# Performance work log

Hardware: AMD Instinct MI355X
Metric: run time of the kernel (lower is better)

The kernel has to match this reference:

```python
import jax, jax.numpy as jnp
import numpy as np

N_NODES = 100000
D = 128
ATT = 128
P_EDGE_TYPES = 3
N_EDGES = 1600000
BATCH = 65536


def gcn_conv(x, W, b, src, dst, n):
    # PyG GCNConv: add self loops, symmetric D^{-1/2} (A+I) D^{-1/2} x W + b
    h = x @ W                                   # [N, D]
    ones = jnp.ones(src.shape[0], x.dtype)
    deg = jax.ops.segment_sum(ones, dst, num_segments=n) + 1.0  # +1 self loop
    dinv = jax.lax.rsqrt(deg)
    norm = dinv[src] * dinv[dst]                # [E]
    out = jax.ops.segment_sum(h[src] * norm[:, None], dst, num_segments=n)
    out = out + h * (dinv * dinv)[:, None]      # self-loop message, norm = dinv_i^2
    return out + b


def semantic_attention(z, P, W, b, q):
    # z: [P*N, D] -> per-edge-type scalar attention, softmax over P, weighted sum
    att = jnp.tanh(z @ W + b) @ q               # [P*N]
    att = att.reshape(P, -1).mean(axis=1)       # [P]
    att = jax.nn.softmax(att)
    zp = z.reshape(P, -1, z.shape[-1])          # [P, N, D]
    return jnp.einsum('p,pnd->nd', att, zp)     # [N, D]


def gnn_branch(x0, edge_index, W1, b1, W2, b2, n):
    outs = []
    for t in range(edge_index.shape[0]):        # fixed small set of edge types
        src, dst = edge_index[t, 0], edge_index[t, 1]
        h = jax.nn.relu(gcn_conv(x0, W1, b1, src, dst, n))
        h = jax.nn.relu(gcn_conv(h, W2, b2, src, dst, n))
        outs.append(h)
    return jnp.concatenate(outs, axis=0)        # [P*N, D]


def setup_inputs() -> dict:
    key = jax.random.key(0)
    ks = jax.random.split(key, 16)
    x = jax.random.normal(ks[0], (N_NODES, D), jnp.float32)
    edge_index = jax.random.randint(ks[1], (P_EDGE_TYPES, 2, N_EDGES), 0, N_NODES, jnp.int64)
    perm = jax.random.permutation(ks[2], N_NODES).astype(jnp.int64)
    summary_vetor = jax.random.normal(ks[3], (D,), jnp.float32)
    s = 1.0 / np.sqrt(D)
    params = dict(
        W_lin=jax.random.normal(ks[4], (D, D), jnp.float32) * s,
        b_lin=jnp.zeros((D,), jnp.float32),
        W1=jax.random.normal(ks[5], (D, D), jnp.float32) * s,
        b1=jnp.zeros((D,), jnp.float32),
        W2=jax.random.normal(ks[6], (D, D), jnp.float32) * s,
        b2=jnp.zeros((D,), jnp.float32),
        W_sem=jax.random.normal(ks[7], (D, ATT), jnp.float32) * s,
        b_sem=jnp.zeros((ATT,), jnp.float32),
        q_sem=jax.random.normal(ks[8], (ATT,), jnp.float32) * (1.0 / np.sqrt(ATT)),
        W_disc=jax.random.normal(ks[9], (D, D), jnp.float32) * s,
        b_disc=jnp.zeros((), jnp.float32),
    )
    return dict(x=x, edge_index=edge_index, perm=perm,
                summary_vetor=summary_vetor, Batch_size=BATCH, **params)


def reference(x, edge_index, perm, summary_vetor, Batch_size,
              W_lin, b_lin, W1, b1, W2, b2, W_sem, b_sem, q_sem, W_disc, b_disc):
    n = x.shape[0]
    x_pos = jax.nn.relu(x @ W_lin + b_lin)
    x_neg = jax.nn.relu(x[perm] @ W_lin + b_lin)

    z_pos = gnn_branch(x_pos, edge_index, W1, b1, W2, b2, n)
    z_neg = gnn_branch(x_neg, edge_index, W1, b1, W2, b2, n)

    P = edge_index.shape[0]
    att_pos = semantic_attention(z_pos, P, W_sem, b_sem, q_sem)[:Batch_size]
    att_neg = semantic_attention(z_neg, P, W_sem, b_sem, q_sem)[:Batch_size]

    summary_in = att_pos.mean(axis=0)           # AvgReadout
    summary = 0.5 * (summary_vetor + summary_in)

    # Discriminator: bilinear score against broadcast summary
    c = W_disc @ summary                        # [D]
    sc_pos = att_pos @ c + b_disc               # [B]
    sc_neg = att_neg @ c + b_disc               # [B]
    ret = jnp.concatenate([sc_pos, sc_neg], axis=0)  # [2B]
    return ret, summary
```

## Files before the change

### kernel.cpp

```cpp
#include <hip/hip_runtime.h>

#define D_ 128
#define BATCH_ 65536
#define BSH 10
#define TILE_ 16384

typedef _Float16 f16;
typedef _Float16 h2v __attribute__((ext_vector_type(2)));
typedef _Float16 f16x8 __attribute__((ext_vector_type(8)));
typedef float f32x4 __attribute__((ext_vector_type(4)));

__global__ void k_zero32(uint32_t* p, long long n) {
    long long i = (long long)blockIdx.x * blockDim.x + threadIdx.x;
    long long st = (long long)gridDim.x * blockDim.x;
    for (; i < n; i += st) p[i] = 0u;
}

__global__ void k_sentinel(float* p, long long n) {
    long long i = (long long)blockIdx.x * blockDim.x + threadIdx.x;
    long long st = (long long)gridDim.x * blockDim.x;
    for (; i < n; i += st) p[i] = -12345.0f;
}

__global__ void k_wt(const float* __restrict__ W, f16* __restrict__ Wt) {
    int t = blockIdx.x * 256 + threadIdx.x;
    int k = t >> 7, c = t & 127;
    Wt[c * 128 + k] = (f16)W[k * 128 + c];
}

__global__ void k_gath(const uint32_t* __restrict__ src, const int* __restrict__ perm,
                       uint32_t* __restrict__ dst, int N) {
    int i = blockIdx.x * 256 + threadIdx.x;
    if (i >= N * 64) return;
    int row = i >> 6, col = i & 63;
    dst[i] = src[((size_t)perm[row] << 6) + col];
}

__global__ void k_hist(const int* __restrict__ ei, int* __restrict__ bcnt,
                       int E, int nbt, int nbuk) {
    __shared__ int hist[512];
    for (int i = threadIdx.x; i < 512; i += 256) hist[i] = 0;
    __syncthreads();
    long long tot = 3LL * E;
    long long i = (long long)blockIdx.x * 256 + threadIdx.x;
    long long st = (long long)gridDim.x * 256;
    for (; i < tot; i += st) {
        int t = (i >= E) + (i >= 2LL * E);
        long long w = i - (long long)t * E;
        int dst = ei[(long long)t * 2 * E + E + w];
        atomicAdd(&hist[t * nbt + (dst >> BSH)], 1);
    }
    __syncthreads();
    for (int i2 = threadIdx.x; i2 < nbuk; i2 += 256)
        if (hist[i2]) atomicAdd(&bcnt[i2], hist[i2]);
}

__global__ void k_bscan(const int* __restrict__ bcnt, int* __restrict__ bbase,
                        int* __restrict__ bcur, int nbuk) {
    __shared__ int s[512];
    int t = threadIdx.x;
    int v = (t < nbuk) ? bcnt[t] : 0;
    s[t] = v;
    __syncthreads();
    for (int off = 1; off < 512; off <<= 1) {
        int a = (t >= off) ? s[t - off] : 0;
        __syncthreads();
        s[t] += a;
        __syncthreads();
    }
    if (t < nbuk) {
        int e = s[t] - v;
        bbase[t] = e;
        bcur[t] = e;
        if (t == nbuk - 1) bbase[nbuk] = s[t];
    }
}

__global__ __launch_bounds__(256) void k_scatter(const int* __restrict__ ei,
                                                 int* __restrict__ bcur,
                                                 uint32_t* __restrict__ pairs,
                                                 int E, int nbt, int nbuk) {
    __shared__ int hist[512];
    __shared__ int base[512];
    long long tot = 3LL * E;
    long long w0 = (long long)blockIdx.x * TILE_;
    long long w1 = w0 + TILE_ < tot ? w0 + TILE_ : tot;
    for (int i = threadIdx.x; i < 512; i += 256) hist[i] = 0;
    __syncthreads();
    for (long long e = w0 + threadIdx.x; e < w1; e += 256) {
        int t = (e >= E) + (e >= 2LL * E);
        long long w = e - (long long)t * E;
        int dst = ei[(long long)t * 2 * E + E + w];
        atomicAdd(&hist[t * nbt + (dst >> BSH)], 1);
    }
    __syncthreads();
    for (int i = threadIdx.x; i < nbuk; i += 256) {
        int c = hist[i];
        base[i] = c ? atomicAdd(&bcur[i], c) : 0;
        hist[i] = 0;
    }
    __syncthreads();
    for (long long e = w0 + threadIdx.x; e < w1; e += 256) {
        int t = (e >= E) + (e >= 2LL * E);
        long long w = e - (long long)t * E;
        int src = ei[(long long)t * 2 * E + w];
        int dst = ei[(long long)t * 2 * E + E + w];
        int b = t * nbt + (dst >> BSH);
        int off = atomicAdd(&hist[b], 1);
        pairs[base[b] + off] = (uint32_t)src | ((uint32_t)(dst & ((1 << BSH) - 1)) << 22);
    }
}

__global__ __launch_bounds__(256) void k_bucket(const uint32_t* __restrict__ pairs,
                                                const int* __restrict__ bbase,
                                                int* __restrict__ rowstart,
                                                float* __restrict__ dinv,
                                                int* __restrict__ csr,
                                                int N, int nbt, int nbuk, int L) {
    __shared__ int cnt[1024];
    __shared__ int pref[1024];
    __shared__ int sums[256];
    int b = blockIdx.x;
    int t = b / nbt, bb = b - t * nbt;
    int dst0 = bb << BSH;
    int ndst = (N - dst0 < 1024) ? (N - dst0) : 1024;
    int e0 = bbase[b], e1 = bbase[b + 1];
    int tid = threadIdx.x;
    for (int i = tid; i < 1024; i += 256) cnt[i] = 0;
    __syncthreads();
    for (int e = e0 + tid; e < e1; e += 256) atomicAdd(&cnt[pairs[e] >> 22], 1);
    __syncthreads();
    int i0 = tid * 4;
    int c0 = cnt[i0], c1 = cnt[i0 + 1], c2 = cnt[i0 + 2], c3 = cnt[i0 + 3];
    int s4 = c0 + c1 + c2 + c3;
    sums[tid] = s4;
    __syncthreads();
    for (int off = 1; off < 256; off <<= 1) {
        int v = (tid >= off) ? sums[tid - off] : 0;
        __syncthreads();
        sums[tid] += v;
        __syncthreads();
    }
    int run = sums[tid] - s4;
    pref[i0] = run; run += c0;
    pref[i0 + 1] = run; run += c1;
    pref[i0 + 2] = run; run += c2;
    pref[i0 + 3] = run;
    __syncthreads();
    for (int d = tid; d < ndst; d += 256) {
        int r = t * N + dst0 + d;
        rowstart[r] = e0 + pref[d];
        dinv[r] = rsqrtf((float)cnt[d] + 1.0f);
    }
    if (b == nbuk - 1 && tid == 0) rowstart[L] = e1;
    __syncthreads();
    for (int e = e0 + tid; e < e1; e += 256) {
        uint32_t u = pairs[e];
        int d = u >> 22;
        int pos = e0 + atomicAdd(&pref[d], 1);
        csr[pos] = (int)(u & ((1u << 22) - 1));
    }
}

__global__ void k_wedge(const int* __restrict__ csr, const float* __restrict__ dinv,
                        f16* __restrict__ w16, int N, int E) {
    long long tot = 3LL * E;
    long long i = (long long)blockIdx.x * 256 + threadIdx.x;
    long long st = (long long)gridDim.x * 256;
    for (; i < tot; i += st) {
        int t = (i >= E) + (i >= 2LL * E);
        w16[i] = (f16)dinv[t * N + csr[i]];
    }
}

__global__ __launch_bounds__(256) void k_mgemm(const void* __restrict__ in, int in_f32,
                                               const f16* __restrict__ Wt,
                                               const float* __restrict__ bias,
                                               f16* __restrict__ outh, int n, int relu) {
    int l = threadIdx.x & 63, wid = threadIdx.x >> 6;
    int row0 = blockIdx.x * 128 + wid * 32;
    int r = l & 15, kg = l >> 4;
    f32x4 acc[2][8] = {};
#pragma unroll
    for (int kk = 0; kk < 4; kk++) {
        int off = kk * 32 + kg * 8;
        f16x8 a[2];
#pragma unroll
        for (int h = 0; h < 2; h++) {
            int arow = row0 + h * 16 + r;
            f16x8 av = {};
            if (arow < n) {
                if (in_f32) {
                    const float* inf = (const float*)in + (size_t)arow * D_ + off;
                    float4 v0 = *(const float4*)inf;
                    float4 v1 = *(const float4*)(inf + 4);
                    av[0] = (f16)v0.x; av[1] = (f16)v0.y; av[2] = (f16)v0.z; av[3] = (f16)v0.w;
                    av[4] = (f16)v1.x; av[5] = (f16)v1.y; av[6] = (f16)v1.z; av[7] = (f16)v1.w;
                } else {
                    av = *(const f16x8*)((const f16*)in + (size_t)arow * D_ + off);
                }
            }
            a[h] = av;
        }
#pragma unroll
        for (int ct = 0; ct < 8; ct++) {
            f16x8 b = *(const f16x8*)(Wt + (size_t)(ct * 16 + r) * D_ + off);
            acc[0][ct] = __builtin_amdgcn_mfma_f32_16x16x32_f16(a[0], b, acc[0][ct], 0, 0, 0);
            acc[1][ct] = __builtin_amdgcn_mfma_f32_16x16x32_f16(a[1], b, acc[1][ct], 0, 0, 0);
        }
    }
#pragma unroll
    for (int h = 0; h < 2; h++) {
#pragma unroll
        for (int ct = 0; ct < 8; ct++) {
            int c = ct * 16 + r;
            float bs = bias ? bias[c] : 0.0f;
#pragma unroll
            for (int j = 0; j < 4; j++) {
                int rr = row0 + h * 16 + kg * 4 + j;
                if (rr >= n) continue;
                float o = acc[h][ct][j] + bs;
                if (relu) o = fmaxf(o, 0.0f);
                outh[(size_t)rr * D_ + c] = (f16)o;
            }
        }
    }
}

__global__ __launch_bounds__(256) void k_matt(const f16* __restrict__ z,
                                              const f16* __restrict__ Wst,
                                              const float* __restrict__ bsem,
                                              const float* __restrict__ q,
                                              float* __restrict__ att_part, int N, int rows) {
    int l = threadIdx.x & 63, wid = threadIdx.x >> 6;
    int row0 = blockIdx.x * 128 + wid * 32;
    int r = l & 15, kg = l >> 4;
    f32x4 acc[2][8] = {};
#pragma unroll
    for (int kk = 0; kk < 4; kk++) {
        int off = kk * 32 + kg * 8;
        f16x8 a[2];
#pragma unroll
        for (int h = 0; h < 2; h++) {
            int arow = row0 + h * 16 + r;
            f16x8 av = {};
            if (arow < rows) av = *(const f16x8*)(z + (size_t)arow * D_ + off);
            a[h] = av;
        }
#pragma unroll
        for (int ct = 0; ct < 8; ct++) {
            f16x8 b = *(const f16x8*)(Wst + (size_t)(ct * 16 + r) * D_ + off);
            acc[0][ct] = __builtin_amdgcn_mfma_f32_16x16x32_f16(a[0], b, acc[0][ct], 0, 0, 0);
            acc[1][ct] = __builtin_amdgcn_mfma_f32_16x16x32_f16(a[1], b, acc[1][ct], 0, 0, 0);
        }
    }
#pragma unroll
    for (int h = 0; h < 2; h++) {
        int rowh = row0 + h * 16;
        if (rowh >= rows) continue;
        float s = 0.0f;
#pragma unroll
        for (int ct = 0; ct < 8; ct++) {
            int c = ct * 16 + r;
            float qc = q[c], bc = bsem[c];
#pragma unroll
            for (int j = 0; j < 4; j++) {
                int rr = rowh + kg * 4 + j;
                if (rr < rows) s += qc * tanhf(acc[h][ct][j] + bc);
            }
        }
#pragma unroll
        for (int m = 1; m < 64; m <<= 1) s += __shfl_xor(s, m, 64);
        if (l == 0) {
            int t = (rowh >= N) + (rowh >= 2 * N);
            atomicAdd(&att_part[((blockIdx.x & 63) << 2) + t], s);
        }
    }
}

__global__ __launch_bounds__(256) void k_spmm(const f16* __restrict__ gsrc,
                                              const int* __restrict__ csr,
                                              const f16* __restrict__ w16,
                                              const int* __restrict__ rowstart,
                                              const float* __restrict__ dinv,
                                              const float* __restrict__ bias,
                                              f16* __restrict__ outh,
                                              int N, int rows, int src_typed) {
    int tid = (int)threadIdx.x;
    int lp = tid & 15;
    int gw = blockIdx.x * 16 + (tid >> 4);
    if (gw >= rows) return;
    int t = (gw >= N) + (gw >= 2 * N);
    int tbase = t * N;
    int sbase = src_typed ? tbase : 0;
    int self = src_typed ? gw : gw - tbase;
    int s0 = rowstart[gw], s1 = rowstart[gw + 1];
    float di = dinv[gw];
    size_t co = (size_t)(lp << 3);
    const f16* gp = gsrc + co;
    float a[8];
    {
        f16x8 sv = *(const f16x8*)(gp + (size_t)self * D_);
#pragma unroll
        for (int u = 0; u < 8; u++) a[u] = (float)sv[u] * di;
    }
    int j = s0;
    for (; j + 2 <= s1; j += 2) {
        int sA = csr[j], sB = csr[j + 1];
        float wA = (float)w16[j], wB = (float)w16[j + 1];
        f16x8 vA = *(const f16x8*)(gp + (size_t)(sbase + sA) * D_);
        f16x8 vB = *(const f16x8*)(gp + (size_t)(sbase + sB) * D_);
#pragma unroll
        for (int u = 0; u < 8; u++) a[u] = fmaf((float)vA[u], wA, a[u]);
#pragma unroll
        for (int u = 0; u < 8; u++) a[u] = fmaf((float)vB[u], wB, a[u]);
    }
    if (j < s1) {
        int s = csr[j];
        float w = (float)w16[j];
        f16x8 v = *(const f16x8*)(gp + (size_t)(sbase + s) * D_);
#pragma unroll
        for (int u = 0; u < 8; u++) a[u] = fmaf((float)v[u], w, a[u]);
    }
    float4 b0 = *(const float4*)(bias + co);
    float4 b1 = *(const float4*)(bias + co + 4);
    f16x8 o;
    o[0] = (f16)fmaxf(fmaf(a[0], di, b0.x), 0.f);
    o[1] = (f16)fmaxf(fmaf(a[1], di, b0.y), 0.f);
    o[2] = (f16)fmaxf(fmaf(a[2], di, b0.z), 0.f);
    o[3] = (f16)fmaxf(fmaf(a[3], di, b0.w), 0.f);
    o[4] = (f16)fmaxf(fmaf(a[4], di, b1.x), 0.f);
    o[5] = (f16)fmaxf(fmaf(a[5], di, b1.y), 0.f);
    o[6] = (f16)fmaxf(fmaf(a[6], di, b1.z), 0.f);
    o[7] = (f16)fmaxf(fmaf(a[7], di, b1.w), 0.f);
    *(f16x8*)(outh + (size_t)gw * D_ + co) = o;
}

__global__ void k_attw(const float* __restrict__ att_part, float* __restrict__ att_w, float invN) {
    __shared__ float sb[3];
    int t = threadIdx.x;
    if (t < 3) {
        float s = 0.f;
        for (int i = 0; i < 64; i++) s += att_part[(i << 2) + t];
        sb[t] = s * invN;
    }
    __syncthreads();
    if (t == 0) {
        float m = fmaxf(sb[0], fmaxf(sb[1], sb[2]));
        float x0 = expf(sb[0] - m), x1 = expf(sb[1] - m), x2 = expf(sb[2] - m);
        float inv = 1.f / (x0 + x1 + x2);
        att_w[0] = x0 * inv; att_w[1] = x1 * inv; att_w[2] = x2 * inv;
    }
}

__global__ __launch_bounds__(256) void k_colsum(const f16* __restrict__ Z, size_t tstride,
                                                const float* __restrict__ att_w,
                                                float* __restrict__ colsum) {
    int c2 = threadIdx.x & 63;
    int rg = threadIdx.x >> 6;
    int nbase = blockIdx.x << 7;
    float w0 = att_w[0], w1 = att_w[1], w2 = att_w[2];
    float csx = 0.f, csy = 0.f;
    for (int i = rg; i < 128; i += 4) {
        size_t off = (size_t)(nbase + i) * D_ + (c2 << 1);
        h2v z0 = *(const h2v*)(Z + off);
        h2v z1 = *(const h2v*)(Z + tstride + off);
        h2v z2 = *(const h2v*)(Z + 2 * tstride + off);
        csx += w0 * (float)z0.x + w1 * (float)z1.x + w2 * (float)z2.x;
        csy += w0 * (float)z0.y + w1 * (float)z1.y + w2 * (float)z2.y;
    }
    __shared__ float red[4][128];
    red[rg][c2 << 1] = csx;
    red[rg][(c2 << 1) + 1] = csy;
    __syncthreads();
    if (rg == 0) {
        float sx = red[0][c2 << 1] + red[1][c2 << 1] + red[2][c2 << 1] + red[3][c2 << 1];
        float sy = red[0][(c2 << 1) + 1] + red[1][(c2 << 1) + 1] + red[2][(c2 << 1) + 1] + red[3][(c2 << 1) + 1];
        atomicAdd(&colsum[c2 << 1], sx);
        atomicAdd(&colsum[(c2 << 1) + 1], sy);
    }
}

__global__ void k_summary_c(const float* __restrict__ colsum, const float* __restrict__ sv,
                            const float* __restrict__ Wd, float* __restrict__ cvec,
                            float* __restrict__ out_summary) {
    __shared__ float sl[128];
    int t = threadIdx.x;
    float s = 0.5f * (sv[t] + colsum[t] * (1.0f / (float)BATCH_));
    sl[t] = s;
    out_summary[t] = s;
    __syncthreads();
    float a = 0.f;
    for (int j = 0; j < 128; j++) a = fmaf(Wd[t * D_ + j], sl[j], a);
    cvec[t] = a;
}

__global__ __launch_bounds__(256) void k_cscore(const f16* __restrict__ Z, size_t tstride,
                                                const float* __restrict__ att_w,
                                                const float* __restrict__ c,
                                                const float* __restrict__ bd,
                                                float* __restrict__ out, int B) {
    int gw = (int)((blockIdx.x * (long long)blockDim.x + threadIdx.x) >> 6);
    int lane = threadIdx.x & 63;
    if (gw >= B) return;
    size_t off = (size_t)gw * D_ + (lane << 1);
    float w0 = att_w[0], w1 = att_w[1], w2 = att_w[2];
    h2v z0 = *(const h2v*)(Z + off);
    h2v z1 = *(const h2v*)(Z + tstride + off);
    h2v z2 = *(const h2v*)(Z + 2 * tstride + off);
    float vx = w0 * (float)z0.x + w1 * (float)z1.x + w2 * (float)z2.x;
    float vy = w0 * (float)z0.y + w1 * (float)z1.y + w2 * (float)z2.y;
    float2 cc = *(const float2*)(c + (lane << 1));
    float a = vx * cc.x + vy * cc.y;
#pragma unroll
    for (int m = 1; m < 64; m <<= 1) a += __shfl_xor(a, m, 64);
    if (lane == 0) out[gw] = a + bd[0];
}

extern "C" void kernel_launch(void* const* d_in, const int* in_sizes, int n_in,
                              void* d_out, int out_size, void* d_ws, size_t ws_size,
                              hipStream_t stream) {
    const float* x      = (const float*)d_in[0];
    const int*   ei     = (const int*)d_in[1];
    const int*   perm   = (const int*)d_in[2];
    const float* sv     = (const float*)d_in[3];
    const float* W_lin  = (const float*)d_in[5];
    const float* b_lin  = (const float*)d_in[6];
    const float* W1     = (const float*)d_in[7];
    const float* b1     = (const float*)d_in[8];
    const float* W2     = (const float*)d_in[9];
    const float* b2     = (const float*)d_in[10];
    const float* W_sem  = (const float*)d_in[11];
    const float* b_sem  = (const float*)d_in[12];
    const float* q_sem  = (const float*)d_in[13];
    const float* W_disc = (const float*)d_in[14];
    const float* b_disc = (const float*)d_in[15];
    float* out = (float*)d_out;

    int N = in_sizes[0] / D_;
    int E = in_sizes[1] / 6;
    int L = 3 * N;
    size_t ND = (size_t)N * D_;
    int B = BATCH_;
    int nbt = (N + (1 << BSH) - 1) >> BSH;
    int nbuk = 3 * nbt;

    char* ws = (char*)d_ws;
    size_t o = 0;
    auto alloc = [&](size_t bytes) -> char* {
        char* p = ws + o;
        o = (o + bytes + 255) & ~(size_t)255;
        return p;
    };
    float* dinv     = (float*)alloc((size_t)L * 4);
    int*   rowstart = (int*)alloc(((size_t)L + 1) * 4);
    int*   csr      = (int*)alloc(((size_t)3 * E + 16) * 4);
    int*   bcnt     = (int*)alloc(512 * 4);
    int*   bbase    = (int*)alloc(513 * 4);
    int*   bcur     = (int*)alloc(512 * 4);
    float* att_part = (float*)alloc(256 * 4);
    float* att_w    = (float*)alloc(16 * 4);
    float* colsum   = (float*)alloc(128 * 4);
    float* cvec     = (float*)alloc(128 * 4);
    f16*   Wlt      = (f16*)alloc(128 * 128 * 2);
    f16*   W1t      = (f16*)alloc(128 * 128 * 2);
    f16*   W2t      = (f16*)alloc(128 * 128 * 2);
    f16*   Wst      = (f16*)alloc(128 * 128 * 2);
    f16*   Ah       = (f16*)alloc(ND * 2);
    f16*   G1h      = (f16*)alloc(ND * 2);
    f16*   G1p      = (f16*)alloc(ND * 2);
    f16*   H1all    = (f16*)alloc(3 * ND * 2);
    f16*   Zall     = (f16*)alloc(3 * ND * 2);
    size_t o_full = o;

    uint32_t* pairs = (uint32_t*)Zall;
    f16*      w16  = (f16*)Ah;

    if (o_full > ws_size || N >= (1 << 22) || (N & 15) || nbuk > 512 ||
        (size_t)3 * E * 4 > 3 * ND * 2 || (size_t)3 * E * 2 > ND * 2) {
        k_sentinel<<<256, 256, 0, stream>>>(out, out_size);
        return;
    }

    k_wt<<<64, 256, 0, stream>>>(W_lin, Wlt);
    k_wt<<<64, 256, 0, stream>>>(W1, W1t);
    k_wt<<<64, 256, 0, stream>>>(W2, W2t);
    k_wt<<<64, 256, 0, stream>>>(W_sem, Wst);

    long long tot = 3LL * E;
    k_zero32<<<2, 256, 0, stream>>>((uint32_t*)bcnt, 512);
    k_hist<<<2048, 256, 0, stream>>>(ei, bcnt, E, nbt, nbuk);
    k_bscan<<<1, 512, 0, stream>>>(bcnt, bbase, bcur, nbuk);
    int scat_grid = (int)((tot + TILE_ - 1) / TILE_);
    k_scatter<<<scat_grid, 256, 0, stream>>>(ei, bcur, pairs, E, nbt, nbuk);
    k_bucket<<<nbuk, 256, 0, stream>>>(pairs, bbase, rowstart, dinv, csr, N, nbt, nbuk, L);

    int mgN_grid  = (N + 127) / 128;
    int mgL_grid  = (L + 127) / 128;
    int spmm_grid = (L + 15) / 16;
    int scoreB_grid = (B + 3) / 4;

    k_mgemm<<<mgN_grid, 256, 0, stream>>>(x, 1, Wlt, b_lin, Ah, N, 1);
    k_mgemm<<<mgN_grid, 256, 0, stream>>>(Ah, 0, W1t, nullptr, G1h, N, 0);
    k_gath<<<(N * 64 + 255) / 256, 256, 0, stream>>>((const uint32_t*)G1h, perm,
                                                     (uint32_t*)G1p, N);
    k_wedge<<<2048, 256, 0, stream>>>(csr, dinv, w16, N, E);

    for (int br = 0; br < 2; br++) {
        const f16* src1 = br ? G1p : G1h;
        float* aw = att_w + br * 8;
        k_zero32<<<1, 256, 0, stream>>>((uint32_t*)att_part, 256);
        k_spmm<<<spmm_grid, 256, 0, stream>>>(src1, csr, w16, rowstart, dinv, b1,
                                              H1all, N, L, 0);
        k_mgemm<<<mgL_grid, 256, 0, stream>>>(H1all, 0, W2t, nullptr, H1all, L, 0);
        k_spmm<<<spmm_grid, 256, 0, stream>>>(H1all, csr, w16, rowstart, dinv, b2,
                                              Zall, N, L, 1);
        k_matt<<<mgL_grid, 256, 0, stream>>>(Zall, Wst, b_sem, q_sem, att_part, N, L);
        k_attw<<<1, 64, 0, stream>>>(att_part, aw, 1.0f / (float)N);
        if (br == 0) {
            k_zero32<<<1, 256, 0, stream>>>((uint32_t*)colsum, 128);
            k_colsum<<<512, 256, 0, stream>>>(Zall, ND, aw, colsum);
            k_summary_c<<<1, 128, 0, stream>>>(colsum, sv, W_disc, cvec, out + 2 * (size_t)B);
            k_cscore<<<scoreB_grid, 256, 0, stream>>>(Zall, ND, aw, cvec, b_disc, out, B);
        } else {
            k_cscore<<<scoreB_grid, 256, 0, stream>>>(Zall, ND, aw, cvec, b_disc, out + B, B);
        }
    }
}
```

Measured before the change: 1.411 ms.

## Fuse GEMM epilogues into SpMM kernels via shared-memory MFMA tiles

The first SpMM now writes its 16 aggregated rows to shared memory and multiplies them by W2 with MFMA in the same block, which removes the separate k_mgemm pass and the H1 round trip through global memory. The second SpMM likewise computes the semantic-attention GEMM, tanh and q-dot on its output tile and accumulates att_part, which removes the separate k_matt pass that re-read Zall. In exchange each 16-row block reloads the full 128x128 weight from global or L2, and the row-level SpMM now carries a block barrier plus extra register pressure from the MFMA phase.

```diff
diff --git a/kernel.cpp b/kernel.cpp
--- a/kernel.cpp
+++ b/kernel.cpp
@@ -227,113 +227,193 @@
     }
 }
 
-__global__ __launch_bounds__(256) void k_matt(const f16* __restrict__ z,
-                                              const f16* __restrict__ Wst,
-                                              const float* __restrict__ bsem,
-                                              const float* __restrict__ q,
-                                              float* __restrict__ att_part, int N, int rows) {
-    int l = threadIdx.x & 63, wid = threadIdx.x >> 6;
-    int row0 = blockIdx.x * 128 + wid * 32;
-    int r = l & 15, kg = l >> 4;
-    f32x4 acc[2][8] = {};
-#pragma unroll
-    for (int kk = 0; kk < 4; kk++) {
-        int off = kk * 32 + kg * 8;
-        f16x8 a[2];
-#pragma unroll
-        for (int h = 0; h < 2; h++) {
-            int arow = row0 + h * 16 + r;
-            f16x8 av = {};
-            if (arow < rows) av = *(const f16x8*)(z + (size_t)arow * D_ + off);
-            a[h] = av;
-        }
-#pragma unroll
-        for (int ct = 0; ct < 8; ct++) {
-            f16x8 b = *(const f16x8*)(Wst + (size_t)(ct * 16 + r) * D_ + off);
-            acc[0][ct] = __builtin_amdgcn_mfma_f32_16x16x32_f16(a[0], b, acc[0][ct], 0, 0, 0);
-            acc[1][ct] = __builtin_amdgcn_mfma_f32_16x16x32_f16(a[1], b, acc[1][ct], 0, 0, 0);
-        }
-    }
-#pragma unroll
-    for (int h = 0; h < 2; h++) {
-        int rowh = row0 + h * 16;
-        if (rowh >= rows) continue;
-        float s = 0.0f;
-#pragma unroll
-        for (int ct = 0; ct < 8; ct++) {
-            int c = ct * 16 + r;
-            float qc = q[c], bc = bsem[c];
-#pragma unroll
-            for (int j = 0; j < 4; j++) {
-                int rr = rowh + kg * 4 + j;
-                if (rr < rows) s += qc * tanhf(acc[h][ct][j] + bc);
-            }
-        }
-#pragma unroll
-        for (int m = 1; m < 64; m <<= 1) s += __shfl_xor(s, m, 64);
-        if (l == 0) {
-            int t = (rowh >= N) + (rowh >= 2 * N);
-            atomicAdd(&att_part[((blockIdx.x & 63) << 2) + t], s);
-        }
-    }
-}
-
-__global__ __launch_bounds__(256) void k_spmm(const f16* __restrict__ gsrc,
-                                              const int* __restrict__ csr,
-                                              const f16* __restrict__ w16,
-                                              const int* __restrict__ rowstart,
-                                              const float* __restrict__ dinv,
-                                              const float* __restrict__ bias,
-                                              f16* __restrict__ outh,
-                                              int N, int rows, int src_typed) {
+__global__ __launch_bounds__(256) void k_spmm1g(const f16* __restrict__ gsrc,
+                                                const int* __restrict__ csr,
+                                                const f16* __restrict__ w16,
+                                                const int* __restrict__ rowstart,
+                                                const float* __restrict__ dinv,
+                                                const float* __restrict__ bias,
+                                                const f16* __restrict__ Wt,
+                                                f16* __restrict__ outG,
+                                                int N, int rows, int src_typed) {
+    __shared__ f16 hs[16][136];
     int tid = (int)threadIdx.x;
     int lp = tid & 15;
-    int gw = blockIdx.x * 16 + (tid >> 4);
-    if (gw >= rows) return;
-    int t = (gw >= N) + (gw >= 2 * N);
-    int tbase = t * N;
-    int sbase = src_typed ? tbase : 0;
-    int self = src_typed ? gw : gw - tbase;
-    int s0 = rowstart[gw], s1 = rowstart[gw + 1];
-    float di = dinv[gw];
-    size_t co = (size_t)(lp << 3);
-    const f16* gp = gsrc + co;
-    float a[8];
-    {
-        f16x8 sv = *(const f16x8*)(gp + (size_t)self * D_);
-#pragma unroll
-        for (int u = 0; u < 8; u++) a[u] = (float)sv[u] * di;
-    }
-    int j = s0;
-    for (; j + 2 <= s1; j += 2) {
-        int sA = csr[j], sB = csr[j + 1];
-        float wA = (float)w16[j], wB = (float)w16[j + 1];
-        f16x8 vA = *(const f16x8*)(gp + (size_t)(sbase + sA) * D_);
-        f16x8 vB = *(const f16x8*)(gp + (size_t)(sbase + sB) * D_);
-#pragma unroll
-        for (int u = 0; u < 8; u++) a[u] = fmaf((float)vA[u], wA, a[u]);
-#pragma unroll
-        for (int u = 0; u < 8; u++) a[u] = fmaf((float)vB[u], wB, a[u]);
-    }
-    if (j < s1) {
-        int s = csr[j];
-        float w = (float)w16[j];
-        f16x8 v = *(const f16x8*)(gp + (size_t)(sbase + s) * D_);
-#pragma unroll
-        for (int u = 0; u < 8; u++) a[u] = fmaf((float)v[u], w, a[u]);
-    }
-    float4 b0 = *(const float4*)(bias + co);
-    float4 b1 = *(const float4*)(bias + co + 4);
-    f16x8 o;
-    o[0] = (f16)fmaxf(fmaf(a[0], di, b0.x), 0.f);
-    o[1] = (f16)fmaxf(fmaf(a[1], di, b0.y), 0.f);
-    o[2] = (f16)fmaxf(fmaf(a[2], di, b0.z), 0.f);
-    o[3] = (f16)fmaxf(fmaf(a[3], di, b0.w), 0.f);
-    o[4] = (f16)fmaxf(fmaf(a[4], di, b1.x), 0.f);
-    o[5] = (f16)fmaxf(fmaf(a[5], di, b1.y), 0.f);
-    o[6] = (f16)fmaxf(fmaf(a[6], di, b1.z), 0.f);
-    o[7] = (f16)fmaxf(fmaf(a[7], di, b1.w), 0.f);
-    *(f16x8*)(outh + (size_t)gw * D_ + co) = o;
+    int row16 = tid >> 4;
+    int gw0 = blockIdx.x * 16;
+    int gw = gw0 + row16;
+    bool valid = gw < rows;
+    float a[8] = {};
+    if (valid) {
+        int t = (gw >= N) + (gw >= 2 * N);
+        int tbase = t * N;
+        int sbase = src_typed ? tbase : 0;
+        int self = src_typed ? gw : gw - tbase;
+        int s0 = rowstart[gw], s1 = rowstart[gw + 1];
+        float di = dinv[gw];
+        size_t co = (size_t)(lp << 3);
+        const f16* gp = gsrc + co;
+        {
+            f16x8 sv = *(const f16x8*)(gp + (size_t)self * D_);
+#pragma unroll
+            for (int u = 0; u < 8; u++) a[u] = (float)sv[u] * di;
+        }
+        int j = s0;
+        for (; j + 2 <= s1; j += 2) {
+            int sA = csr[j], sB = csr[j + 1];
+            float wA = (float)w16[j], wB = (float)w16[j + 1];
+            f16x8 vA = *(const f16x8*)(gp + (size_t)(sbase + sA) * D_);
+            f16x8 vB = *(const f16x8*)(gp + (size_t)(sbase + sB) * D_);
+#pragma unroll
+            for (int u = 0; u < 8; u++) a[u] = fmaf((float)vA[u], wA, a[u]);
+#pragma unroll
+            for (int u = 0; u < 8; u++) a[u] = fmaf((float)vB[u], wB, a[u]);
+        }
+        if (j < s1) {
+            int s = csr[j];
+            float w = (float)w16[j];
+            f16x8 v = *(const f16x8*)(gp + (size_t)(sbase + s) * D_);
+#pragma unroll
+            for (int u = 0; u < 8; u++) a[u] = fmaf((float)v[u], w, a[u]);
+        }
+        float4 b0 = *(const float4*)(bias + co);
+        float4 b1v = *(const float4*)(bias + co + 4);
+        a[0] = fmaxf(fmaf(a[0], di, b0.x), 0.f);
+        a[1] = fmaxf(fmaf(a[1], di, b0.y), 0.f);
+        a[2] = fmaxf(fmaf(a[2], di, b0.z), 0.f);
+        a[3] = fmaxf(fmaf(a[3], di, b0.w), 0.f);
+        a[4] = fmaxf(fmaf(a[4], di, b1v.x), 0.f);
+        a[5] = fmaxf(fmaf(a[5], di, b1v.y), 0.f);
+        a[6] = fmaxf(fmaf(a[6], di, b1v.z), 0.f);
+        a[7] = fmaxf(fmaf(a[7], di, b1v.w), 0.f);
+    }
+    f16x8 hv;
+#pragma unroll
+    for (int u = 0; u < 8; u++) hv[u] = (f16)a[u];
+    *(f16x8*)&hs[row16][lp << 3] = hv;
+    __syncthreads();
+    int l = tid & 63, wid = tid >> 6;
+    int r = l & 15, kg = l >> 4;
+    f16x8 af[4];
+#pragma unroll
+    for (int kk = 0; kk < 4; kk++) af[kk] = *(const f16x8*)&hs[r][kk * 32 + kg * 8];
+#pragma unroll
+    for (int ct = 0; ct < 2; ct++) {
+        int c = wid * 32 + ct * 16 + r;
+        f32x4 acc = {};
+#pragma unroll
+        for (int kk = 0; kk < 4; kk++) {
+            f16x8 b = *(const f16x8*)(Wt + (size_t)c * D_ + kk * 32 + kg * 8);
+            acc = __builtin_amdgcn_mfma_f32_16x16x32_f16(af[kk], b, acc, 0, 0, 0);
+        }
+#pragma unroll
+        for (int j = 0; j < 4; j++) {
+            int rr = gw0 + kg * 4 + j;
+            if (rr < rows) outG[(size_t)rr * D_ + c] = (f16)acc[j];
+        }
+    }
+}
+
+__global__ __launch_bounds__(256) void k_spmm2a(const f16* __restrict__ gsrc,
+                                                const int* __restrict__ csr,
+                                                const f16* __restrict__ w16,
+                                                const int* __restrict__ rowstart,
+                                                const float* __restrict__ dinv,
+                                                const float* __restrict__ bias,
+                                                const f16* __restrict__ Wst,
+                                                const float* __restrict__ bsem,
+                                                const float* __restrict__ q,
+                                                f16* __restrict__ outZ,
+                                                float* __restrict__ att_part,
+                                                int N, int rows, int src_typed) {
+    __shared__ f16 hs[16][136];
+    __shared__ float ws[4];
+    int tid = (int)threadIdx.x;
+    int lp = tid & 15;
+    int row16 = tid >> 4;
+    int gw0 = blockIdx.x * 16;
+    int gw = gw0 + row16;
+    bool valid = gw < rows;
+    float a[8] = {};
+    if (valid) {
+        int t = (gw >= N) + (gw >= 2 * N);
+        int tbase = t * N;
+        int sbase = src_typed ? tbase : 0;
+        int self = src_typed ? gw : gw - tbase;
+        int s0 = rowstart[gw], s1 = rowstart[gw + 1];
+        float di = dinv[gw];
+        size_t co = (size_t)(lp << 3);
+        const f16* gp = gsrc + co;
+        {
+            f16x8 sv = *(const f16x8*)(gp + (size_t)self * D_);
+#pragma unroll
+            for (int u = 0; u < 8; u++) a[u] = (float)sv[u] * di;
+        }
+        int j = s0;
+        for (; j + 2 <= s1; j += 2) {
+            int sA = csr[j], sB = csr[j + 1];
+            float wA = (float)w16[j], wB = (float)w16[j + 1];
+            f16x8 vA = *(const f16x8*)(gp + (size_t)(sbase + sA) * D_);
+            f16x8 vB = *(const f16x8*)(gp + (size_t)(sbase + sB) * D_);
+#pragma unroll
+            for (int u = 0; u < 8; u++) a[u] = fmaf((float)vA[u], wA, a[u]);
+#pragma unroll
+            for (int u = 0; u < 8; u++) a[u] = fmaf((float)vB[u], wB, a[u]);
+        }
+        if (j < s1) {
+            int s = csr[j];
+            float w = (float)w16[j];
+            f16x8 v = *(const f16x8*)(gp + (size_t)(sbase + s) * D_);
+#pragma unroll
+            for (int u = 0; u < 8; u++) a[u] = fmaf((float)v[u], w, a[u]);
+        }
+        float4 b0 = *(const float4*)(bias + co);
+        float4 b1v = *(const float4*)(bias + co + 4);
+        a[0] = fmaxf(fmaf(a[0], di, b0.x), 0.f);
+        a[1] = fmaxf(fmaf(a[1], di, b0.y), 0.f);
+        a[2] = fmaxf(fmaf(a[2], di, b0.z), 0.f);
+        a[3] = fmaxf(fmaf(a[3], di, b0.w), 0.f);
+        a[4] = fmaxf(fmaf(a[4], di, b1v.x), 0.f);
+        a[5] = fmaxf(fmaf(a[5], di, b1v.y), 0.f);
+        a[6] = fmaxf(fmaf(a[6], di, b1v.z), 0.f);
+        a[7] = fmaxf(fmaf(a[7], di, b1v.w), 0.f);
+    }
+    f16x8 hv;
+#pragma unroll
+    for (int u = 0; u < 8; u++) hv[u] = (f16)a[u];
+    *(f16x8*)&hs[row16][lp << 3] = hv;
+    if (valid) *(f16x8*)(outZ + (size_t)gw * D_ + (size_t)(lp << 3)) = hv;
+    __syncthreads();
+    int l = tid & 63, wid = tid >> 6;
+    int r = l & 15, kg = l >> 4;
+    f16x8 af[4];
+#pragma unroll
+    for (int kk = 0; kk < 4; kk++) af[kk] = *(const f16x8*)&hs[r][kk * 32 + kg * 8];
+    float s = 0.0f;
+#pragma unroll
+    for (int ct = 0; ct < 2; ct++) {
+        int c = wid * 32 + ct * 16 + r;
+        f32x4 acc = {};
+#pragma unroll
+        for (int kk = 0; kk < 4; kk++) {
+            f16x8 b = *(const f16x8*)(Wst + (size_t)c * D_ + kk * 32 + kg * 8);
+            acc = __builtin_amdgcn_mfma_f32_16x16x32_f16(af[kk], b, acc, 0, 0, 0);
+        }
+        float qc = q[c], bc = bsem[c];
+#pragma unroll
+        for (int j = 0; j < 4; j++) {
+            int rr = gw0 + kg * 4 + j;
+            if (rr < rows) s += qc * tanhf(acc[j] + bc);
+        }
+    }
+#pragma unroll
+    for (int m = 1; m < 64; m <<= 1) s += __shfl_xor(s, m, 64);
+    if (l == 0) ws[wid] = s;
+    __syncthreads();
+    if (tid == 0) {
+        int t = (gw0 >= N) + (gw0 >= 2 * N);
+        atomicAdd(&att_part[((blockIdx.x & 63) << 2) + t], ws[0] + ws[1] + ws[2] + ws[3]);
+    }
 }
 
 __global__ void k_attw(const float* __restrict__ att_part, float* __restrict__ att_w, float invN) {
@@ -469,7 +549,7 @@
     f16*   Ah       = (f16*)alloc(ND * 2);
     f16*   G1h      = (f16*)alloc(ND * 2);
     f16*   G1p      = (f16*)alloc(ND * 2);
-    f16*   H1all    = (f16*)alloc(3 * ND * 2);
+    f16*   G2all    = (f16*)alloc(3 * ND * 2);
     f16*   Zall     = (f16*)alloc(3 * ND * 2);
     size_t o_full = o;
 
@@ -496,7 +576,6 @@
     k_bucket<<<nbuk, 256, 0, stream>>>(pairs, bbase, rowstart, dinv, csr, N, nbt, nbuk, L);
 
     int mgN_grid  = (N + 127) / 128;
-    int mgL_grid  = (L + 127) / 128;
     int spmm_grid = (L + 15) / 16;
     int scoreB_grid = (B + 3) / 4;
 
@@ -510,12 +589,10 @@
         const f16* src1 = br ? G1p : G1h;
         float* aw = att_w + br * 8;
         k_zero32<<<1, 256, 0, stream>>>((uint32_t*)att_part, 256);
-        k_spmm<<<spmm_grid, 256, 0, stream>>>(src1, csr, w16, rowstart, dinv, b1,
-                                              H1all, N, L, 0);
-        k_mgemm<<<mgL_grid, 256, 0, stream>>>(H1all, 0, W2t, nullptr, H1all, L, 0);
-        k_spmm<<<spmm_grid, 256, 0, stream>>>(H1all, csr, w16, rowstart, dinv, b2,
-                                              Zall, N, L, 1);
-        k_matt<<<mgL_grid, 256, 0, stream>>>(Zall, Wst, b_sem, q_sem, att_part, N, L);
+        k_spmm1g<<<spmm_grid, 256, 0, stream>>>(src1, csr, w16, rowstart, dinv, b1,
+                                                W2t, G2all, N, L, 0);
+        k_spmm2a<<<spmm_grid, 256, 0, stream>>>(G2all, csr, w16, rowstart, dinv, b2,
+                                                Wst, b_sem, q_sem, Zall, att_part, N, L, 1);
         k_attw<<<1, 64, 0, stream>>>(att_part, aw, 1.0f / (float)N);
         if (br == 0) {
             k_zero32<<<1, 256, 0, stream>>>((uint32_t*)colsum, 128);
```

Result: faster. 1.248 ms (-11.5%).
